# Kernel optimization log

Measured on AMD Instinct MI355X. Metric: run time of the kernel, lower is better.

Reference implementation:

```python
import jax, jax.numpy as jnp
import numpy as np

# SH constants (standard 3DGS eval_sh, degree 3)
C0 = 0.28209479177387814
C1 = 0.4886025119029199
C2 = (1.0925484305920792, -1.0925484305920792, 0.31539156525252005, -1.0925484305920792, 0.5462742152960396)
C3 = (-0.5900435899266435, 2.890611442640554, -0.4570457994644658, 0.3731763325901154, -0.4570457994644658, 1.445305721320277, -0.5900435899266435)

N_GAUSS = 4096
N_PTS = 32768
CHUNK = 4096  # math-identical to torch's 16384 chunking (pure concat of independent points)


def quat_to_rot(q):
    # q: (N,4) normalized, (w,x,y,z) as in 3DGS build_rotation
    r, x, y, z = q[:, 0], q[:, 1], q[:, 2], q[:, 3]
    R = jnp.stack([
        jnp.stack([1 - 2 * (y * y + z * z), 2 * (x * y - r * z), 2 * (x * z + r * y)], -1),
        jnp.stack([2 * (x * y + r * z), 1 - 2 * (x * x + z * z), 2 * (y * z - r * x)], -1),
        jnp.stack([2 * (x * z - r * y), 2 * (y * z + r * x), 1 - 2 * (x * x + y * y)], -1),
    ], axis=-2)  # (N,3,3)
    return R


def eval_sh3(sh, dirs):
    # sh: (N,16) scalar SH coeffs; dirs: (C,N,3) unit directions -> (C,N)
    x, y, z = dirs[..., 0], dirs[..., 1], dirs[..., 2]
    xx, yy, zz = x * x, y * y, z * z
    xy, yz, xz = x * y, y * z, x * z
    s = sh[None]  # (1,N,16)
    res = C0 * s[..., 0]
    res = res - C1 * y * s[..., 1] + C1 * z * s[..., 2] - C1 * x * s[..., 3]
    res = (res + C2[0] * xy * s[..., 4] + C2[1] * yz * s[..., 5]
           + C2[2] * (2 * zz - xx - yy) * s[..., 6]
           + C2[3] * xz * s[..., 7] + C2[4] * (xx - yy) * s[..., 8])
    res = (res + C3[0] * y * (3 * xx - yy) * s[..., 9] + C3[1] * xy * z * s[..., 10]
           + C3[2] * y * (4 * zz - xx - yy) * s[..., 11]
           + C3[3] * z * (2 * zz - 3 * xx - 3 * yy) * s[..., 12]
           + C3[4] * x * (4 * zz - xx - yy) * s[..., 13]
           + C3[5] * z * (xx - yy) * s[..., 14]
           + C3[6] * x * (xx - yy - 3 * zz) * s[..., 15])
    return res


def setup_inputs() -> dict:
    key = jax.random.key(0)
    ks = jax.random.split(key, 9)
    return {
        "network_pts": jax.random.normal(ks[0], (N_PTS, 3), jnp.float32),
        "network_view": jax.random.normal(ks[1], (N_PTS, 3), jnp.float32),
        "network_tx": jax.random.normal(ks[2], (N_PTS, 3), jnp.float32),
        "xyz": jax.random.normal(ks[3], (N_GAUSS, 3), jnp.float32),
        "sh_dc": jax.random.normal(ks[4], (N_GAUSS, 1), jnp.float32),
        "sh_rest": 0.1 * jax.random.normal(ks[5], (N_GAUSS, 15), jnp.float32),
        "scaling": jnp.float32(-3.0) + 0.2 * jax.random.normal(ks[6], (N_GAUSS, 3), jnp.float32),
        "rotation": jax.random.normal(ks[7], (N_GAUSS, 4), jnp.float32),
        "opacity_logit": jax.random.normal(ks[8], (N_GAUSS, 1), jnp.float32),
    }


def reference(network_pts, network_view, network_tx, xyz, sh_dc, sh_rest, scaling, rotation, opacity_logit):
    # activations, matching GaussianModel.setup_functions
    sh = jnp.concatenate([sh_dc, sh_rest], axis=1)            # (N,16)
    s = jnp.exp(scaling)                                      # (N,3)
    q = rotation / jnp.linalg.norm(rotation, axis=1, keepdims=True)
    R = quat_to_rot(q)                                        # (N,3,3)
    # precision = (L L^T)^{-1} with L = R diag(s)  =>  R diag(1/s^2) R^T
    prec = jnp.einsum('nij,nj,nkj->nik', R, 1.0 / (s * s), R)  # (N,3,3)
    op = jax.nn.sigmoid(opacity_logit)[:, 0]                  # (N,)

    pts = network_pts.reshape(-1, CHUNK, 3)

    def chunk_fn(p):  # p: (C,3)
        diff = p[:, None, :] - xyz[None, :, :]                # (C,N,3)
        maha = jnp.einsum('cni,nij,cnj->cn', diff, prec, diff)
        w = op[None, :] * jnp.exp(-0.5 * maha)                # (C,N)
        # dir_pp = xyz - query_point, normalized (as in get_magnitude)
        dirs = -diff / jnp.linalg.norm(diff, axis=-1, keepdims=True)
        mag = jnp.maximum(eval_sh3(sh, dirs), 0.0)            # (C,N)
        return w.sum(axis=1), (w * mag).sum(axis=1)

    opac_c, sig_c = jax.lax.map(chunk_fn, pts)
    return opac_c.reshape(-1), sig_c.reshape(-1)
```

## Files before the change

kernel.cpp:

```cpp
#include <hip/hip_runtime.h>
#include <hip/hip_bf16.h>

#define N_GAUSS 4096
#define N_PTS   32768
#define BLOCK   256
#define NSPLIT  32
#define SEGSZ   (N_GAUSS / NSPLIT)
#define NBLK_PT 128
#define GSTRIDE 28
#define NCELL   4096

#define SH_C0  0.28209479177387814f
#define SH_C1  0.4886025119029199f

#define WS_GP     0
#define WS_GHIST  114688
#define WS_CELLID 118784
#define WS_SPTS   151552
#define WS_PART   282624

__device__ __forceinline__ int expand4(int b) {
    return (b & 1) | ((b & 2) << 2) | ((b & 4) << 4) | ((b & 8) << 6);
}

__global__ __launch_bounds__(256) void prep_bin_kernel(
    const float* __restrict__ pts, const float* __restrict__ xyz,
    const float* __restrict__ sh_dc, const float* __restrict__ sh_rest,
    const float* __restrict__ scaling, const float* __restrict__ rotation,
    const float* __restrict__ opl, float* __restrict__ gp, int* __restrict__ cellid)
{
    const int tid = threadIdx.x, bx = blockIdx.x;
    if (bx < 16) {
        int g = bx * 256 + tid;
        float s0 = scaling[3*g+0], s1 = scaling[3*g+1], s2 = scaling[3*g+2];
        float i0 = __expf(-2.0f * s0);
        float i1 = __expf(-2.0f * s1);
        float i2 = __expf(-2.0f * s2);
        float maxs2 = __expf(2.0f * fmaxf(s0, fmaxf(s1, s2)));

        float r = rotation[4*g+0], x = rotation[4*g+1];
        float y = rotation[4*g+2], z = rotation[4*g+3];
        float n = rsqrtf(r*r + x*x + y*y + z*z);
        r *= n; x *= n; y *= n; z *= n;
        float R00 = 1.f - 2.f*(y*y + z*z), R01 = 2.f*(x*y - r*z), R02 = 2.f*(x*z + r*y);
        float R10 = 2.f*(x*y + r*z), R11 = 1.f - 2.f*(x*x + z*z), R12 = 2.f*(y*z - r*x);
        float R20 = 2.f*(x*z - r*y), R21 = 2.f*(y*z + r*x), R22 = 1.f - 2.f*(x*x + y*y);

        float pxx = 0.5f*(R00*R00*i0 + R01*R01*i1 + R02*R02*i2);
        float pxy = 0.5f*(R00*R10*i0 + R01*R11*i1 + R02*R12*i2);
        float pxz = 0.5f*(R00*R20*i0 + R01*R21*i1 + R02*R22*i2);
        float pyy = 0.5f*(R10*R10*i0 + R11*R11*i1 + R12*R12*i2);
        float pyz = 0.5f*(R10*R20*i0 + R11*R21*i1 + R12*R22*i2);
        float pzz = 0.5f*(R20*R20*i0 + R21*R21*i1 + R22*R22*i2);

        float op    = 1.f / (1.f + __expf(-opl[g]));
        float lnop  = __logf(op);
        float Tg    = 2.0f * maxs2 * (lnop + 16.0f);

        float* G = gp + (size_t)g * GSTRIDE;
        G[0] = xyz[3*g+0]; G[1] = xyz[3*g+1]; G[2] = xyz[3*g+2]; G[3] = Tg;
        G[4] = pxx; G[5] = pxy; G[6] = pxz; G[7] = pyy; G[8] = pyz; G[9] = pzz;
        G[10] = lnop; G[11] = 0.f;

        const float* sr = sh_rest + (size_t)g * 15;
        G[12] =  SH_C0 * sh_dc[g];
        G[13] = -SH_C1 * sr[0];
        G[14] =  SH_C1 * sr[1];
        G[15] = -SH_C1 * sr[2];
        G[16] =  1.0925484305920792f  * sr[3];
        G[17] = -1.0925484305920792f  * sr[4];
        G[18] =  0.31539156525252005f * sr[5];
        G[19] = -1.0925484305920792f  * sr[6];
        G[20] =  0.5462742152960396f  * sr[7];
        G[21] = -0.5900435899266435f  * sr[8];
        G[22] =  2.890611442640554f   * sr[9];
        G[23] = -0.4570457994644658f  * sr[10];
        G[24] =  0.3731763325901154f  * sr[11];
        G[25] = -0.4570457994644658f  * sr[12];
        G[26] =  1.445305721320277f   * sr[13];
        G[27] = -0.5900435899266435f  * sr[14];
    } else {
        int p = (bx - 16) * 256 + tid;
        float x = pts[3*p+0], y = pts[3*p+1], z = pts[3*p+2];
        int cx = min(15, max(0, (int)((x + 3.2f) * 2.5f)));
        int cy = min(15, max(0, (int)((y + 3.2f) * 2.5f)));
        int cz = min(15, max(0, (int)((z + 3.2f) * 2.5f)));
        cellid[p] = expand4(cx) | (expand4(cy) << 1) | (expand4(cz) << 2);
    }
}

__global__ __launch_bounds__(1024) void scan_kernel(
    const int* __restrict__ cellid, int* __restrict__ ghist)
{
    __shared__ int s_hist[NCELL];
    __shared__ int s_scan[1024];
    const int t = threadIdx.x;
    #pragma unroll
    for (int i = 0; i < 4; ++i) s_hist[t + i * 1024] = 0;
    __syncthreads();
    for (int p = t; p < N_PTS; p += 1024) atomicAdd(&s_hist[cellid[p]], 1);
    __syncthreads();
    int b = t * 4;
    int c0 = s_hist[b], c1 = s_hist[b+1], c2 = s_hist[b+2], c3 = s_hist[b+3];
    int s = c0 + c1 + c2 + c3;
    s_scan[t] = s;
    __syncthreads();
    for (int off = 1; off < 1024; off <<= 1) {
        int v = (t >= off) ? s_scan[t - off] : 0;
        __syncthreads();
        s_scan[t] += v;
        __syncthreads();
    }
    int excl = s_scan[t] - s;
    ghist[b]   = excl;
    ghist[b+1] = excl + c0;
    ghist[b+2] = excl + c0 + c1;
    ghist[b+3] = excl + c0 + c1 + c2;
}

__global__ __launch_bounds__(256) void scatter_kernel(
    const float* __restrict__ pts, const int* __restrict__ cellid,
    int* __restrict__ ghist, float4* __restrict__ spts)
{
    int p = blockIdx.x * 256 + threadIdx.x;
    float x = pts[3*p+0], y = pts[3*p+1], z = pts[3*p+2];
    int pos = atomicAdd(&ghist[cellid[p]], 1);
    spts[pos] = make_float4(x, y, z, __int_as_float(p));
}

__device__ __forceinline__ void eval_one(
    const float* __restrict__ G, float dx, float dy, float dz, float d2,
    float& opac, float& sig)
{
    float vx = G[4]*dx + G[5]*dy + G[6]*dz;
    float vy = G[5]*dx + G[7]*dy + G[8]*dz;
    float vz = G[6]*dx + G[8]*dy + G[9]*dz;
    float maha = dx*vx + dy*vy + dz*vz;
    float w = __expf(G[10] - maha);
    opac += w;

    if (__any(w > 1e-9f)) {
        float rinv = rsqrtf(d2);
        float x = -dx * rinv, y = -dy * rinv, z = -dz * rinv;
        float xx = x*x, yy = y*y, zz = z*z;
        float xy = x*y, yz = y*z, xz = x*z;

        float res = G[12];
        res += y * G[13];
        res += z * G[14];
        res += x * G[15];
        res += xy * G[16];
        res += yz * G[17];
        res += (3.f*zz - 1.f) * G[18];
        res += xz * G[19];
        float xxmyy = xx - yy;
        res += xxmyy * G[20];
        res += y * (3.f*xx - yy) * G[21];
        res += (xy * z) * G[22];
        float f5z1 = 5.f*zz - 1.f;
        res += y * f5z1 * G[23];
        res += z * (5.f*zz - 3.f) * G[24];
        res += x * f5z1 * G[25];
        res += z * xxmyy * G[26];
        res += x * (xxmyy - 3.f*zz) * G[27];

        sig += w * fmaxf(res, 0.f);
    }
}

__global__ __launch_bounds__(BLOCK, 4) void gauss_kernel(
    const float4* __restrict__ spts, const float* __restrict__ gp,
    float2* __restrict__ part)
{
    __shared__ float s_min[4][3], s_max[4][3];
    __shared__ int s_nact;
    __shared__ int s_act[SEGSZ];

    const int tid = threadIdx.x;
    const int pb  = blockIdx.x;
    const int seg = blockIdx.y;
    float4 P = spts[pb * 256 + tid];
    const float px = P.x, py = P.y, pz = P.z;

    float mnx = px, mxx = px, mny = py, mxy = py, mnz = pz, mxz = pz;
    #pragma unroll
    for (int off = 32; off >= 1; off >>= 1) {
        mnx = fminf(mnx, __shfl_xor(mnx, off));
        mxx = fmaxf(mxx, __shfl_xor(mxx, off));
        mny = fminf(mny, __shfl_xor(mny, off));
        mxy = fmaxf(mxy, __shfl_xor(mxy, off));
        mnz = fminf(mnz, __shfl_xor(mnz, off));
        mxz = fmaxf(mxz, __shfl_xor(mxz, off));
    }
    const int wave = tid >> 6;
    if ((tid & 63) == 0) {
        s_min[wave][0] = mnx; s_min[wave][1] = mny; s_min[wave][2] = mnz;
        s_max[wave][0] = mxx; s_max[wave][1] = mxy; s_max[wave][2] = mxz;
    }
    if (tid == 0) s_nact = 0;
    __syncthreads();
    const float bmnx = fminf(fminf(s_min[0][0], s_min[1][0]), fminf(s_min[2][0], s_min[3][0]));
    const float bmny = fminf(fminf(s_min[0][1], s_min[1][1]), fminf(s_min[2][1], s_min[3][1]));
    const float bmnz = fminf(fminf(s_min[0][2], s_min[1][2]), fminf(s_min[2][2], s_min[3][2]));
    const float bmxx = fmaxf(fmaxf(s_max[0][0], s_max[1][0]), fmaxf(s_max[2][0], s_max[3][0]));
    const float bmxy = fmaxf(fmaxf(s_max[0][1], s_max[1][1]), fmaxf(s_max[2][1], s_max[3][1]));
    const float bmxz = fmaxf(fmaxf(s_max[0][2], s_max[1][2]), fmaxf(s_max[2][2], s_max[3][2]));

    if (tid < SEGSZ) {
        const int gg = seg * SEGSZ + tid;
        const float* Gc = gp + (size_t)gg * GSTRIDE;
        float cx = Gc[0], cy = Gc[1], cz = Gc[2], Tg = Gc[3];
        float ddx = fmaxf(0.f, fmaxf(bmnx - cx, cx - bmxx));
        float ddy = fmaxf(0.f, fmaxf(bmny - cy, cy - bmxy));
        float ddz = fmaxf(0.f, fmaxf(bmnz - cz, cz - bmxz));
        float dd2 = ddx*ddx + ddy*ddy + ddz*ddz;
        if (dd2 <= Tg) {
            int slot = atomicAdd(&s_nact, 1);
            s_act[slot] = gg;
        }
    }
    __syncthreads();
    const int nact = s_nact;

    float opac = 0.f, sig = 0.f;
    for (int j = 0; j < nact; j += 2) {
        const bool has1 = (j + 1 < nact);
        const int g0 = __builtin_amdgcn_readfirstlane(s_act[j]);
        const int g1 = __builtin_amdgcn_readfirstlane(s_act[has1 ? j + 1 : j]);
        const float* __restrict__ A = gp + (size_t)g0 * GSTRIDE;
        const float* __restrict__ B = gp + (size_t)g1 * GSTRIDE;

        float a0 = A[0], a1 = A[1], a2 = A[2], aT = A[3];
        float b0 = B[0], b1 = B[1], b2 = B[2], bT = B[3];
        float adx = px - a0, ady = py - a1, adz = pz - a2;
        float bdx = px - b0, bdy = py - b1, bdz = pz - b2;
        float ad2 = adx*adx + ady*ady + adz*adz;
        float bd2 = bdx*bdx + bdy*bdy + bdz*bdz;

        if (!__all(ad2 > aT)) eval_one(A, adx, ady, adz, ad2, opac, sig);
        if (has1 && !__all(bd2 > bT)) eval_one(B, bdx, bdy, bdz, bd2, opac, sig);
    }

    part[((size_t)(pb * NSPLIT + seg)) * 256 + tid] = make_float2(opac, sig);
}

__global__ __launch_bounds__(256) void reduce_kernel(
    const float2* __restrict__ part, const float4* __restrict__ spts,
    float* __restrict__ out)
{
    const int tid = threadIdx.x, pb = blockIdx.x;
    float o = 0.f, sg = 0.f;
    #pragma unroll
    for (int s = 0; s < NSPLIT; ++s) {
        float2 v = part[((size_t)(pb * NSPLIT + s)) * 256 + tid];
        o += v.x; sg += v.y;
    }
    int orig = __float_as_int(spts[pb * 256 + tid].w);
    out[orig] = o;
    out[N_PTS + orig] = sg;
}

extern "C" void kernel_launch(void* const* d_in, const int* in_sizes, int n_in,
                              void* d_out, int out_size, void* d_ws, size_t ws_size,
                              hipStream_t stream) {
    const float* pts      = (const float*)d_in[0];
    const float* xyz      = (const float*)d_in[3];
    const float* sh_dc    = (const float*)d_in[4];
    const float* sh_rest  = (const float*)d_in[5];
    const float* scaling  = (const float*)d_in[6];
    const float* rotation = (const float*)d_in[7];
    const float* opl      = (const float*)d_in[8];

    float*  out    = (float*)d_out;
    float*  wsf    = (float*)d_ws;
    float*  gp     = wsf + WS_GP;
    int*    ghist  = (int*)(wsf + WS_GHIST);
    int*    cellid = (int*)(wsf + WS_CELLID);
    float4* spts   = (float4*)(wsf + WS_SPTS);
    float2* part   = (float2*)(wsf + WS_PART);

    prep_bin_kernel<<<dim3(144), dim3(256), 0, stream>>>(
        pts, xyz, sh_dc, sh_rest, scaling, rotation, opl, gp, cellid);
    scan_kernel<<<dim3(1), dim3(1024), 0, stream>>>(cellid, ghist);
    scatter_kernel<<<dim3(NBLK_PT), dim3(256), 0, stream>>>(pts, cellid, ghist, spts);

    dim3 grid(NBLK_PT, NSPLIT);
    gauss_kernel<<<grid, dim3(BLOCK), 0, stream>>>(spts, gp, part);
    reduce_kernel<<<dim3(NBLK_PT), dim3(256), 0, stream>>>(part, spts, out);
}
```

Baseline: 130.9 us.

## Merge scan into scatter, cull per 64-point slice, reduce in-block

The single-block scan kernel is removed. Every scatter block now rebuilds the full cell histogram and prefix sum in shared memory, and per-cell cursors that the prep kernel zeroes give each point its slot. The gauss kernel now gives each block 64 sorted points and all 4096 Gaussians. Each wave culls against its own 64-point bounding box and the four waves split the active list, with partials summed in shared memory and written straight to the output. This drops the split-by-segment grid, the partial buffer and the reduce kernel, cutting launches and global traffic, at the cost of redundant histogram work in every scatter block and a more serial per-block loop over active Gaussians.

```diff
diff --git a/kernel.cpp b/kernel.cpp
--- a/kernel.cpp
+++ b/kernel.cpp
@@ -3,21 +3,17 @@
 
 #define N_GAUSS 4096
 #define N_PTS   32768
-#define BLOCK   256
-#define NSPLIT  32
-#define SEGSZ   (N_GAUSS / NSPLIT)
-#define NBLK_PT 128
 #define GSTRIDE 28
 #define NCELL   4096
+#define NSLICE  512
 
 #define SH_C0  0.28209479177387814f
 #define SH_C1  0.4886025119029199f
 
 #define WS_GP     0
-#define WS_GHIST  114688
+#define WS_GCUR   114688
 #define WS_CELLID 118784
 #define WS_SPTS   151552
-#define WS_PART   282624
 
 __device__ __forceinline__ int expand4(int b) {
     return (b & 1) | ((b & 2) << 2) | ((b & 4) << 4) | ((b & 8) << 6);
@@ -27,10 +23,13 @@
     const float* __restrict__ pts, const float* __restrict__ xyz,
     const float* __restrict__ sh_dc, const float* __restrict__ sh_rest,
     const float* __restrict__ scaling, const float* __restrict__ rotation,
-    const float* __restrict__ opl, float* __restrict__ gp, int* __restrict__ cellid)
+    const float* __restrict__ opl, float* __restrict__ gp,
+    int* __restrict__ cellid, int* __restrict__ gcursor)
 {
     const int tid = threadIdx.x, bx = blockIdx.x;
     if (bx < 16) {
+        gcursor[bx * 256 + tid] = 0;
+
         int g = bx * 256 + tid;
         float s0 = scaling[3*g+0], s1 = scaling[3*g+1], s2 = scaling[3*g+2];
         float i0 = __expf(-2.0f * s0);
@@ -53,9 +52,9 @@
         float pyz = 0.5f*(R10*R20*i0 + R11*R21*i1 + R12*R22*i2);
         float pzz = 0.5f*(R20*R20*i0 + R21*R21*i1 + R22*R22*i2);
 
-        float op    = 1.f / (1.f + __expf(-opl[g]));
-        float lnop  = __logf(op);
-        float Tg    = 2.0f * maxs2 * (lnop + 16.0f);
+        float op   = 1.f / (1.f + __expf(-opl[g]));
+        float lnop = __logf(op);
+        float Tg   = 2.0f * maxs2 * (lnop + 16.0f);
 
         float* G = gp + (size_t)g * GSTRIDE;
         G[0] = xyz[3*g+0]; G[1] = xyz[3*g+1]; G[2] = xyz[3*g+2]; G[3] = Tg;
@@ -89,42 +88,43 @@
     }
 }
 
-__global__ __launch_bounds__(1024) void scan_kernel(
-    const int* __restrict__ cellid, int* __restrict__ ghist)
-{
-    __shared__ int s_hist[NCELL];
-    __shared__ int s_scan[1024];
-    const int t = threadIdx.x;
-    #pragma unroll
-    for (int i = 0; i < 4; ++i) s_hist[t + i * 1024] = 0;
-    __syncthreads();
-    for (int p = t; p < N_PTS; p += 1024) atomicAdd(&s_hist[cellid[p]], 1);
-    __syncthreads();
-    int b = t * 4;
-    int c0 = s_hist[b], c1 = s_hist[b+1], c2 = s_hist[b+2], c3 = s_hist[b+3];
-    int s = c0 + c1 + c2 + c3;
-    s_scan[t] = s;
-    __syncthreads();
-    for (int off = 1; off < 1024; off <<= 1) {
-        int v = (t >= off) ? s_scan[t - off] : 0;
+__global__ __launch_bounds__(256) void scanscatter_kernel(
+    const float* __restrict__ pts, const int* __restrict__ cellid,
+    int* __restrict__ gcursor, float4* __restrict__ spts)
+{
+    __shared__ int s_start[NCELL];
+    __shared__ int s_red[256];
+    const int tid = threadIdx.x, bx = blockIdx.x;
+
+    #pragma unroll
+    for (int i = 0; i < 16; ++i) s_start[tid + i * 256] = 0;
+    __syncthreads();
+    #pragma unroll 4
+    for (int i = 0; i < 128; ++i)
+        atomicAdd(&s_start[cellid[i * 256 + tid]], 1);
+    __syncthreads();
+
+    int base = tid * 16;
+    int c[16]; int tot = 0;
+    #pragma unroll
+    for (int i = 0; i < 16; ++i) { c[i] = s_start[base + i]; tot += c[i]; }
+    s_red[tid] = tot;
+    __syncthreads();
+    for (int off = 1; off < 256; off <<= 1) {
+        int v = (tid >= off) ? s_red[tid - off] : 0;
         __syncthreads();
-        s_scan[t] += v;
+        s_red[tid] += v;
         __syncthreads();
     }
-    int excl = s_scan[t] - s;
-    ghist[b]   = excl;
-    ghist[b+1] = excl + c0;
-    ghist[b+2] = excl + c0 + c1;
-    ghist[b+3] = excl + c0 + c1 + c2;
-}
-
-__global__ __launch_bounds__(256) void scatter_kernel(
-    const float* __restrict__ pts, const int* __restrict__ cellid,
-    int* __restrict__ ghist, float4* __restrict__ spts)
-{
-    int p = blockIdx.x * 256 + threadIdx.x;
+    int run = s_red[tid] - tot;
+    #pragma unroll
+    for (int i = 0; i < 16; ++i) { int cc = c[i]; s_start[base + i] = run; run += cc; }
+    __syncthreads();
+
+    int p = bx * 256 + tid;
     float x = pts[3*p+0], y = pts[3*p+1], z = pts[3*p+2];
-    int pos = atomicAdd(&ghist[cellid[p]], 1);
+    int cell = cellid[p];
+    int pos  = s_start[cell] + atomicAdd(&gcursor[cell], 1);
     spts[pos] = make_float4(x, y, z, __int_as_float(p));
 }
 
@@ -168,19 +168,22 @@
     }
 }
 
-__global__ __launch_bounds__(BLOCK, 4) void gauss_kernel(
+__global__ __launch_bounds__(256, 4) void gauss_kernel(
     const float4* __restrict__ spts, const float* __restrict__ gp,
-    float2* __restrict__ part)
-{
-    __shared__ float s_min[4][3], s_max[4][3];
+    float* __restrict__ out)
+{
     __shared__ int s_nact;
-    __shared__ int s_act[SEGSZ];
-
-    const int tid = threadIdx.x;
-    const int pb  = blockIdx.x;
-    const int seg = blockIdx.y;
-    float4 P = spts[pb * 256 + tid];
+    __shared__ int s_act[N_GAUSS];
+    __shared__ float s_part[4][64][2];
+
+    const int tid  = threadIdx.x;
+    const int lane = tid & 63;
+    const int wv   = tid >> 6;
+    const int bx   = blockIdx.x;
+
+    float4 P = spts[bx * 64 + lane];
     const float px = P.x, py = P.y, pz = P.z;
+    const int orig = __float_as_int(P.w);
 
     float mnx = px, mxx = px, mny = py, mxy = py, mnz = pz, mxz = pz;
     #pragma unroll
@@ -192,41 +195,31 @@
         mnz = fminf(mnz, __shfl_xor(mnz, off));
         mxz = fmaxf(mxz, __shfl_xor(mxz, off));
     }
-    const int wave = tid >> 6;
-    if ((tid & 63) == 0) {
-        s_min[wave][0] = mnx; s_min[wave][1] = mny; s_min[wave][2] = mnz;
-        s_max[wave][0] = mxx; s_max[wave][1] = mxy; s_max[wave][2] = mxz;
-    }
+
     if (tid == 0) s_nact = 0;
     __syncthreads();
-    const float bmnx = fminf(fminf(s_min[0][0], s_min[1][0]), fminf(s_min[2][0], s_min[3][0]));
-    const float bmny = fminf(fminf(s_min[0][1], s_min[1][1]), fminf(s_min[2][1], s_min[3][1]));
-    const float bmnz = fminf(fminf(s_min[0][2], s_min[1][2]), fminf(s_min[2][2], s_min[3][2]));
-    const float bmxx = fmaxf(fmaxf(s_max[0][0], s_max[1][0]), fmaxf(s_max[2][0], s_max[3][0]));
-    const float bmxy = fmaxf(fmaxf(s_max[0][1], s_max[1][1]), fmaxf(s_max[2][1], s_max[3][1]));
-    const float bmxz = fmaxf(fmaxf(s_max[0][2], s_max[1][2]), fmaxf(s_max[2][2], s_max[3][2]));
-
-    if (tid < SEGSZ) {
-        const int gg = seg * SEGSZ + tid;
-        const float* Gc = gp + (size_t)gg * GSTRIDE;
-        float cx = Gc[0], cy = Gc[1], cz = Gc[2], Tg = Gc[3];
-        float ddx = fmaxf(0.f, fmaxf(bmnx - cx, cx - bmxx));
-        float ddy = fmaxf(0.f, fmaxf(bmny - cy, cy - bmxy));
-        float ddz = fmaxf(0.f, fmaxf(bmnz - cz, cz - bmxz));
+
+    #pragma unroll 4
+    for (int i = 0; i < 16; ++i) {
+        const int g = i * 256 + tid;
+        const float4 c = *(const float4*)(gp + (size_t)g * GSTRIDE);
+        float ddx = fmaxf(0.f, fmaxf(mnx - c.x, c.x - mxx));
+        float ddy = fmaxf(0.f, fmaxf(mny - c.y, c.y - mxy));
+        float ddz = fmaxf(0.f, fmaxf(mnz - c.z, c.z - mxz));
         float dd2 = ddx*ddx + ddy*ddy + ddz*ddz;
-        if (dd2 <= Tg) {
+        if (dd2 <= c.w) {
             int slot = atomicAdd(&s_nact, 1);
-            s_act[slot] = gg;
+            s_act[slot] = g;
         }
     }
     __syncthreads();
     const int nact = s_nact;
 
     float opac = 0.f, sig = 0.f;
-    for (int j = 0; j < nact; j += 2) {
-        const bool has1 = (j + 1 < nact);
+    for (int j = wv; j < nact; j += 8) {
+        const bool has1 = (j + 4 < nact);
         const int g0 = __builtin_amdgcn_readfirstlane(s_act[j]);
-        const int g1 = __builtin_amdgcn_readfirstlane(s_act[has1 ? j + 1 : j]);
+        const int g1 = __builtin_amdgcn_readfirstlane(s_act[has1 ? j + 4 : j]);
         const float* __restrict__ A = gp + (size_t)g0 * GSTRIDE;
         const float* __restrict__ B = gp + (size_t)g1 * GSTRIDE;
 
@@ -241,23 +234,18 @@
         if (has1 && !__all(bd2 > bT)) eval_one(B, bdx, bdy, bdz, bd2, opac, sig);
     }
 
-    part[((size_t)(pb * NSPLIT + seg)) * 256 + tid] = make_float2(opac, sig);
-}
-
-__global__ __launch_bounds__(256) void reduce_kernel(
-    const float2* __restrict__ part, const float4* __restrict__ spts,
-    float* __restrict__ out)
-{
-    const int tid = threadIdx.x, pb = blockIdx.x;
-    float o = 0.f, sg = 0.f;
-    #pragma unroll
-    for (int s = 0; s < NSPLIT; ++s) {
-        float2 v = part[((size_t)(pb * NSPLIT + s)) * 256 + tid];
-        o += v.x; sg += v.y;
-    }
-    int orig = __float_as_int(spts[pb * 256 + tid].w);
-    out[orig] = o;
-    out[N_PTS + orig] = sg;
+    s_part[wv][lane][0] = opac;
+    s_part[wv][lane][1] = sig;
+    __syncthreads();
+
+    if (tid < 64) {
+        float o  = s_part[0][tid][0] + s_part[1][tid][0]
+                 + s_part[2][tid][0] + s_part[3][tid][0];
+        float sg = s_part[0][tid][1] + s_part[1][tid][1]
+                 + s_part[2][tid][1] + s_part[3][tid][1];
+        out[orig] = o;
+        out[N_PTS + orig] = sg;
+    }
 }
 
 extern "C" void kernel_launch(void* const* d_in, const int* in_sizes, int n_in,
@@ -271,20 +259,16 @@
     const float* rotation = (const float*)d_in[7];
     const float* opl      = (const float*)d_in[8];
 
-    float*  out    = (float*)d_out;
-    float*  wsf    = (float*)d_ws;
-    float*  gp     = wsf + WS_GP;
-    int*    ghist  = (int*)(wsf + WS_GHIST);
-    int*    cellid = (int*)(wsf + WS_CELLID);
-    float4* spts   = (float4*)(wsf + WS_SPTS);
-    float2* part   = (float2*)(wsf + WS_PART);
+    float*  out     = (float*)d_out;
+    float*  wsf     = (float*)d_ws;
+    float*  gp      = wsf + WS_GP;
+    int*    gcursor = (int*)(wsf + WS_GCUR);
+    int*    cellid  = (int*)(wsf + WS_CELLID);
+    float4* spts    = (float4*)(wsf + WS_SPTS);
 
     prep_bin_kernel<<<dim3(144), dim3(256), 0, stream>>>(
-        pts, xyz, sh_dc, sh_rest, scaling, rotation, opl, gp, cellid);
-    scan_kernel<<<dim3(1), dim3(1024), 0, stream>>>(cellid, ghist);
-    scatter_kernel<<<dim3(NBLK_PT), dim3(256), 0, stream>>>(pts, cellid, ghist, spts);
-
-    dim3 grid(NBLK_PT, NSPLIT);
-    gauss_kernel<<<grid, dim3(BLOCK), 0, stream>>>(spts, gp, part);
-    reduce_kernel<<<dim3(NBLK_PT), dim3(256), 0, stream>>>(part, spts, out);
-}
+        pts, xyz, sh_dc, sh_rest, scaling, rotation, opl, gp, cellid, gcursor);
+    scanscatter_kernel<<<dim3(128), dim3(256), 0, stream>>>(
+        pts, cellid, gcursor, spts);
+    gauss_kernel<<<dim3(NSLICE), dim3(256), 0, stream>>>(spts, gp, out);
+}
```

Result: slower. 249.3 us (+90.4%).

## Fuse binning histogram, scan and scatter into one redundant-histogram setup kernel

Applied to the files above, without the earlier changes.

Replaces the separate prep, single-block scan and atomic scatter kernels with one setup kernel. Each point block redundantly builds the full cell histogram of all points in shared memory, scans it locally, and computes deterministic scatter positions from a prefix count plus an in-block rank. This removes two kernel launches and the serialized single-block scan. In exchange every block reads all point coordinates and does 32K shared atomics, and each thread runs an O(tid) rank loop.

```diff
diff --git a/kernel.cpp b/kernel.cpp
--- a/kernel.cpp
+++ b/kernel.cpp
@@ -13,25 +13,31 @@
 #define SH_C0  0.28209479177387814f
 #define SH_C1  0.4886025119029199f
 
-#define WS_GP     0
-#define WS_GHIST  114688
-#define WS_CELLID 118784
-#define WS_SPTS   151552
-#define WS_PART   282624
-
-__device__ __forceinline__ int expand4(int b) {
-    return (b & 1) | ((b & 2) << 2) | ((b & 4) << 4) | ((b & 8) << 6);
-}
-
-__global__ __launch_bounds__(256) void prep_bin_kernel(
+#define WS_GP   0
+#define WS_SPTS 114688
+#define WS_PART 245760
+
+__device__ __forceinline__ int cell_of(float x, float y, float z) {
+    int cx = min(15, max(0, (int)((x + 3.2f) * 2.5f)));
+    int cy = min(15, max(0, (int)((y + 3.2f) * 2.5f)));
+    int cz = min(15, max(0, (int)((z + 3.2f) * 2.5f)));
+    int ex = (cx & 1) | ((cx & 2) << 2) | ((cx & 4) << 4) | ((cx & 8) << 6);
+    int ey = (cy & 1) | ((cy & 2) << 2) | ((cy & 4) << 4) | ((cy & 8) << 6);
+    int ez = (cz & 1) | ((cz & 2) << 2) | ((cz & 4) << 4) | ((cz & 8) << 6);
+    return ex | (ey << 1) | (ez << 2);
+}
+
+__global__ __launch_bounds__(256) void setup_kernel(
     const float* __restrict__ pts, const float* __restrict__ xyz,
     const float* __restrict__ sh_dc, const float* __restrict__ sh_rest,
     const float* __restrict__ scaling, const float* __restrict__ rotation,
-    const float* __restrict__ opl, float* __restrict__ gp, int* __restrict__ cellid)
+    const float* __restrict__ opl, float* __restrict__ gp,
+    float4* __restrict__ spts)
 {
     const int tid = threadIdx.x, bx = blockIdx.x;
-    if (bx < 16) {
-        int g = bx * 256 + tid;
+
+    if (bx >= NBLK_PT) {
+        int g = (bx - NBLK_PT) * 256 + tid;
         float s0 = scaling[3*g+0], s1 = scaling[3*g+1], s2 = scaling[3*g+2];
         float i0 = __expf(-2.0f * s0);
         float i1 = __expf(-2.0f * s1);
@@ -53,9 +59,9 @@
         float pyz = 0.5f*(R10*R20*i0 + R11*R21*i1 + R12*R22*i2);
         float pzz = 0.5f*(R20*R20*i0 + R21*R21*i1 + R22*R22*i2);
 
-        float op    = 1.f / (1.f + __expf(-opl[g]));
-        float lnop  = __logf(op);
-        float Tg    = 2.0f * maxs2 * (lnop + 16.0f);
+        float op   = 1.f / (1.f + __expf(-opl[g]));
+        float lnop = __logf(op);
+        float Tg   = 2.0f * maxs2 * (lnop + 16.0f);
 
         float* G = gp + (size_t)g * GSTRIDE;
         G[0] = xyz[3*g+0]; G[1] = xyz[3*g+1]; G[2] = xyz[3*g+2]; G[3] = Tg;
@@ -79,53 +85,59 @@
         G[25] = -0.4570457994644658f  * sr[12];
         G[26] =  1.445305721320277f   * sr[13];
         G[27] = -0.5900435899266435f  * sr[14];
-    } else {
-        int p = (bx - 16) * 256 + tid;
+        return;
+    }
+
+    __shared__ int s_start[NCELL];
+    __shared__ int s_pre[NCELL];
+    __shared__ int s_red[256];
+    __shared__ unsigned short s_mycell[256];
+
+    #pragma unroll
+    for (int i = 0; i < 16; ++i) {
+        s_start[tid + i * 256] = 0;
+        s_pre[tid + i * 256]   = 0;
+    }
+    __syncthreads();
+
+    float myx = 0.f, myy = 0.f, myz = 0.f;
+    int mycell = 0;
+    for (int k = 0; k < NBLK_PT; ++k) {
+        int p = k * 256 + tid;
         float x = pts[3*p+0], y = pts[3*p+1], z = pts[3*p+2];
-        int cx = min(15, max(0, (int)((x + 3.2f) * 2.5f)));
-        int cy = min(15, max(0, (int)((y + 3.2f) * 2.5f)));
-        int cz = min(15, max(0, (int)((z + 3.2f) * 2.5f)));
-        cellid[p] = expand4(cx) | (expand4(cy) << 1) | (expand4(cz) << 2);
-    }
-}
-
-__global__ __launch_bounds__(1024) void scan_kernel(
-    const int* __restrict__ cellid, int* __restrict__ ghist)
-{
-    __shared__ int s_hist[NCELL];
-    __shared__ int s_scan[1024];
-    const int t = threadIdx.x;
-    #pragma unroll
-    for (int i = 0; i < 4; ++i) s_hist[t + i * 1024] = 0;
-    __syncthreads();
-    for (int p = t; p < N_PTS; p += 1024) atomicAdd(&s_hist[cellid[p]], 1);
-    __syncthreads();
-    int b = t * 4;
-    int c0 = s_hist[b], c1 = s_hist[b+1], c2 = s_hist[b+2], c3 = s_hist[b+3];
-    int s = c0 + c1 + c2 + c3;
-    s_scan[t] = s;
-    __syncthreads();
-    for (int off = 1; off < 1024; off <<= 1) {
-        int v = (t >= off) ? s_scan[t - off] : 0;
+        int cell = cell_of(x, y, z);
+        atomicAdd(&s_start[cell], 1);
+        if (k < bx) atomicAdd(&s_pre[cell], 1);
+        if (k == bx) {
+            myx = x; myy = y; myz = z; mycell = cell;
+            s_mycell[tid] = (unsigned short)cell;
+        }
+    }
+    __syncthreads();
+
+    int base = tid * 16;
+    int c[16]; int tot = 0;
+    #pragma unroll
+    for (int i = 0; i < 16; ++i) { c[i] = s_start[base + i]; tot += c[i]; }
+    s_red[tid] = tot;
+    __syncthreads();
+    for (int off = 1; off < 256; off <<= 1) {
+        int v = (tid >= off) ? s_red[tid - off] : 0;
         __syncthreads();
-        s_scan[t] += v;
+        s_red[tid] += v;
         __syncthreads();
     }
-    int excl = s_scan[t] - s;
-    ghist[b]   = excl;
-    ghist[b+1] = excl + c0;
-    ghist[b+2] = excl + c0 + c1;
-    ghist[b+3] = excl + c0 + c1 + c2;
-}
-
-__global__ __launch_bounds__(256) void scatter_kernel(
-    const float* __restrict__ pts, const int* __restrict__ cellid,
-    int* __restrict__ ghist, float4* __restrict__ spts)
-{
-    int p = blockIdx.x * 256 + threadIdx.x;
-    float x = pts[3*p+0], y = pts[3*p+1], z = pts[3*p+2];
-    int pos = atomicAdd(&ghist[cellid[p]], 1);
-    spts[pos] = make_float4(x, y, z, __int_as_float(p));
+    int run = s_red[tid] - tot;
+    #pragma unroll
+    for (int i = 0; i < 16; ++i) { int cc = c[i]; s_start[base + i] = run; run += cc; }
+    __syncthreads();
+
+    int rank = 0;
+    for (int t2 = 0; t2 < tid; ++t2) rank += (s_mycell[t2] == (unsigned short)mycell);
+
+    int p_mine = bx * 256 + tid;
+    int pos = s_start[mycell] + s_pre[mycell] + rank;
+    spts[pos] = make_float4(myx, myy, myz, __int_as_float(p_mine));
 }
 
 __device__ __forceinline__ void eval_one(
@@ -271,18 +283,14 @@
     const float* rotation = (const float*)d_in[7];
     const float* opl      = (const float*)d_in[8];
 
-    float*  out    = (float*)d_out;
-    float*  wsf    = (float*)d_ws;
-    float*  gp     = wsf + WS_GP;
-    int*    ghist  = (int*)(wsf + WS_GHIST);
-    int*    cellid = (int*)(wsf + WS_CELLID);
-    float4* spts   = (float4*)(wsf + WS_SPTS);
-    float2* part   = (float2*)(wsf + WS_PART);
-
-    prep_bin_kernel<<<dim3(144), dim3(256), 0, stream>>>(
-        pts, xyz, sh_dc, sh_rest, scaling, rotation, opl, gp, cellid);
-    scan_kernel<<<dim3(1), dim3(1024), 0, stream>>>(cellid, ghist);
-    scatter_kernel<<<dim3(NBLK_PT), dim3(256), 0, stream>>>(pts, cellid, ghist, spts);
+    float*  out  = (float*)d_out;
+    float*  wsf  = (float*)d_ws;
+    float*  gp   = wsf + WS_GP;
+    float4* spts = (float4*)(wsf + WS_SPTS);
+    float2* part = (float2*)(wsf + WS_PART);
+
+    setup_kernel<<<dim3(NBLK_PT + 16), dim3(256), 0, stream>>>(
+        pts, xyz, sh_dc, sh_rest, scaling, rotation, opl, gp, spts);
 
     dim3 grid(NBLK_PT, NSPLIT);
     gauss_kernel<<<grid, dim3(BLOCK), 0, stream>>>(spts, gp, part);
```

After: 157.7 us. 20.4% more time.
